# Optimization experiments

Measured on AMD Instinct MI355X. Metric: run time of the kernel, lower is better.

## Reference

```python
import jax, jax.numpy as jnp
import numpy as np

N_NODES = 50000
N_EDGES = 640000
IN_DIM = 128
HID = 128
G_OUT = 128
AX_IN = 64
AX_OUT = 64
OUT_CH = 8
N_GRAPHS = 512


def gcn_conv(x, W, b, src, dst, norm, n_nodes):
    # PyG GCNConv: out = scatter_add(norm * (x W)[src] -> dst) + b
    h = x @ W  # [N, F_out]
    msg = h[src] * norm[:, None]  # [E', F_out]
    return jax.ops.segment_sum(msg, dst, num_segments=n_nodes) + b


def setup_inputs() -> dict:
    key = jax.random.key(0)
    ks = jax.random.split(key, 16)
    inp = {}
    inp["x"] = jax.random.normal(ks[0], (N_NODES, IN_DIM), dtype=jnp.float32)
    inp["edge_index"] = jax.random.randint(ks[1], (2, N_EDGES), 0, N_NODES, dtype=jnp.int64)
    inp["batch"] = jnp.sort(jax.random.randint(ks[2], (N_NODES,), 0, N_GRAPHS, dtype=jnp.int64))
    inp["ax_data"] = jax.random.normal(ks[3], (N_GRAPHS, AX_IN), dtype=jnp.float32)
    def lin(k, fi, fo):
        s = 1.0 / np.sqrt(fi)
        k1, k2 = jax.random.split(k)
        return (jax.random.uniform(k1, (fi, fo), jnp.float32, -s, s),
                jax.random.uniform(k2, (fo,), jnp.float32, -s, s))
    inp["W1"], inp["b1"] = lin(ks[4], IN_DIM, HID)
    inp["W2"], inp["b2"] = lin(ks[5], HID, HID)
    inp["lin1_W"], inp["lin1_b"] = lin(ks[6], HID, G_OUT)
    inp["ax_W"], inp["ax_b"] = lin(ks[7], AX_IN, AX_OUT)
    inp["lin2_W"], inp["lin2_b"] = lin(ks[8], G_OUT + AX_OUT, OUT_CH)
    return inp


def reference(x, edge_index, batch, ax_data, W1, b1, W2, b2, lin1_W, lin1_b, ax_W, ax_b, lin2_W, lin2_b):
    n_nodes = x.shape[0]
    n_graphs = ax_data.shape[0]
    # add self-loops (PyG GCNConv default add_self_loops=True)
    loop = jnp.arange(n_nodes, dtype=edge_index.dtype)
    src = jnp.concatenate([edge_index[0], loop])
    dst = jnp.concatenate([edge_index[1], loop])
    # symmetric normalization D^-1/2 (A+I) D^-1/2
    deg = jax.ops.segment_sum(jnp.ones_like(dst, dtype=x.dtype), dst, num_segments=n_nodes)
    dinv = jax.lax.rsqrt(jnp.maximum(deg, 1.0))  # deg >= 1 with self-loops
    norm = dinv[src] * dinv[dst]  # [E+N]

    h = jax.nn.relu(gcn_conv(x, W1, b1, src, dst, norm, n_nodes))
    h = jax.nn.relu(gcn_conv(h, W2, b2, src, dst, norm, n_nodes))

    # global_mean_pool over batch ids
    sums = jax.ops.segment_sum(h, batch, num_segments=n_graphs)
    cnts = jax.ops.segment_sum(jnp.ones((n_nodes,), h.dtype), batch, num_segments=n_graphs)
    pooled = sums / jnp.maximum(cnts, 1.0)[:, None]  # [G, HID]

    g = pooled @ lin1_W + lin1_b            # [G, G_OUT]
    a = ax_data @ ax_W + ax_b               # [G, AX_OUT]
    z = jnp.concatenate([g, a], axis=1)     # [G, G_OUT+AX_OUT]
    return z @ lin2_W + lin2_b              # [G, OUT_CH]
```

## Files before the change

kernel.cpp:

```cpp
#include <hip/hip_runtime.h>


#define ELLCAP 62
#define BCAP 2048

typedef __attribute__((ext_vector_type(8))) short bf16x8;
typedef __attribute__((ext_vector_type(4))) float f32x4;
typedef __attribute__((ext_vector_type(2))) float f32x2;

static __device__ __forceinline__ unsigned short f2bf(float f) {
  unsigned u = __float_as_uint(f);
  return (unsigned short)((u + 0x7fffu + ((u >> 16) & 1u)) >> 16);
}
static __device__ __forceinline__ unsigned pack2(float a, float b) {
  return (unsigned)f2bf(a) | ((unsigned)f2bf(b) << 16);
}
static __device__ __forceinline__ unsigned char f2fp8(float v) {
  return (unsigned char)(__builtin_amdgcn_cvt_pk_fp8_f32(v, 0.f, 0, false) & 0xff);
}
static __device__ __forceinline__ unsigned enc2(float a, float b) {
  return __builtin_amdgcn_cvt_pk_fp8_f32(a, b, 0, false) & 0xffffu;
}
static __device__ __forceinline__ void add16(float* a, uint4 h) {
  f32x2 t;
  t = __builtin_amdgcn_cvt_pk_f32_fp8(h.x, false); a[0] += t[0]; a[1] += t[1];
  t = __builtin_amdgcn_cvt_pk_f32_fp8(h.x, true);  a[2] += t[0]; a[3] += t[1];
  t = __builtin_amdgcn_cvt_pk_f32_fp8(h.y, false); a[4] += t[0]; a[5] += t[1];
  t = __builtin_amdgcn_cvt_pk_f32_fp8(h.y, true);  a[6] += t[0]; a[7] += t[1];
  t = __builtin_amdgcn_cvt_pk_f32_fp8(h.z, false); a[8] += t[0]; a[9] += t[1];
  t = __builtin_amdgcn_cvt_pk_f32_fp8(h.z, true);  a[10] += t[0]; a[11] += t[1];
  t = __builtin_amdgcn_cvt_pk_f32_fp8(h.w, false); a[12] += t[0]; a[13] += t[1];
  t = __builtin_amdgcn_cvt_pk_f32_fp8(h.w, true);  a[14] += t[0]; a[15] += t[1];
}
static __device__ __forceinline__ uint4 scale16(uint4 h, float d) {
  f32x2 t; float v[16];
  t = __builtin_amdgcn_cvt_pk_f32_fp8(h.x, false); v[0] = d * t[0]; v[1] = d * t[1];
  t = __builtin_amdgcn_cvt_pk_f32_fp8(h.x, true);  v[2] = d * t[0]; v[3] = d * t[1];
  t = __builtin_amdgcn_cvt_pk_f32_fp8(h.y, false); v[4] = d * t[0]; v[5] = d * t[1];
  t = __builtin_amdgcn_cvt_pk_f32_fp8(h.y, true);  v[6] = d * t[0]; v[7] = d * t[1];
  t = __builtin_amdgcn_cvt_pk_f32_fp8(h.z, false); v[8] = d * t[0]; v[9] = d * t[1];
  t = __builtin_amdgcn_cvt_pk_f32_fp8(h.z, true);  v[10] = d * t[0]; v[11] = d * t[1];
  t = __builtin_amdgcn_cvt_pk_f32_fp8(h.w, false); v[12] = d * t[0]; v[13] = d * t[1];
  t = __builtin_amdgcn_cvt_pk_f32_fp8(h.w, true);  v[14] = d * t[0]; v[15] = d * t[1];
  uint4 r;
  r.x = enc2(v[0], v[1]) | (enc2(v[2], v[3]) << 16);
  r.y = enc2(v[4], v[5]) | (enc2(v[6], v[7]) << 16);
  r.z = enc2(v[8], v[9]) | (enc2(v[10], v[11]) << 16);
  r.w = enc2(v[12], v[13]) | (enc2(v[14], v[15]) << 16);
  return r;
}

__global__ void k_wprep(const float* __restrict__ W1, const float* __restrict__ W2,
                        unsigned short* __restrict__ wt1, unsigned short* __restrict__ wt2,
                        unsigned* __restrict__ gcnt, int nb) {
  int b = blockIdx.x, t = threadIdx.x;
  if (b < 128) {
    int idx = b * 256 + t;
    int w = idx >> 14, r = (idx >> 7) & 127, kk = idx & 127;
    if (w == 0) wt1[r * 128 + kk] = f2bf(W1[kk * 128 + r]);
    else        wt2[r * 128 + kk] = f2bf(W2[kk * 128 + r]);
  } else {
    int i = (b - 128) * 256 + t;
    if (i < nb) gcnt[i * 32] = 0;
  }
}

__global__ __launch_bounds__(256, 4) void k_mega1(
    const float* __restrict__ X, const uint4* __restrict__ WT4,
    unsigned char* __restrict__ H8,
    const int* __restrict__ srcv, const int* __restrict__ dstv,
    unsigned* __restrict__ gcnt, unsigned* __restrict__ packed,
    int E, int M, int NG) {
  __shared__ __align__(16) unsigned short sW[64 * 136];
  __shared__ __align__(16) unsigned short sX[64 * 136];
  __shared__ unsigned sbin[392];
  __shared__ unsigned sbase[392];
  int b = blockIdx.x, t = threadIdx.x;
  if (b < NG) {
    int m0 = b * 64;
    const float4* X4 = (const float4*)X;
#pragma unroll
    for (int r = 0; r < 8; r++) {
      int idx = t + r * 256;
      int rr = idx >> 5, c4 = idx & 31;
      int m = m0 + rr;
      float4 v = make_float4(0.f, 0.f, 0.f, 0.f);
      if (m < M) v = X4[(size_t)m * 32 + c4];
      unsigned short* pp = sX + rr * 136 + c4 * 4;
      *(ushort2*)(pp) = make_ushort2(f2bf(v.x), f2bf(v.y));
      *(ushort2*)(pp + 2) = make_ushort2(f2bf(v.z), f2bf(v.w));
    }
    int lane = t & 63, wv = t >> 6;
    int ln15 = lane & 15, q = lane >> 4;
    int r0 = m0 + wv * 16 + q * 4;
    bf16x8 afrag[4];
#pragma unroll
    for (int half = 0; half < 2; half++) {
      if (half) __syncthreads();
#pragma unroll
      for (int r = 0; r < 4; r++) {
        int idx = t + r * 256;
        int nn = idx >> 4, c8 = idx & 15;
        *(uint4*)(sW + nn * 136 + c8 * 8) = WT4[(half * 64 + nn) * 16 + c8];
      }
      __syncthreads();
      if (half == 0) {
#pragma unroll
        for (int c = 0; c < 4; c++)
          afrag[c] = *(const bf16x8*)(sX + (wv * 16 + ln15) * 136 + c * 32 + q * 8);
      }
#pragma unroll
      for (int jj = 0; jj < 4; jj++) {
        int j = half * 4 + jj;
        f32x4 acc = {0.f, 0.f, 0.f, 0.f};
#pragma unroll
        for (int c = 0; c < 4; c++) {
          bf16x8 bfrag = *(const bf16x8*)(sW + (jj * 16 + ln15) * 136 + c * 32 + q * 8);
          acc = __builtin_amdgcn_mfma_f32_16x16x32_bf16(afrag[c], bfrag, acc, 0, 0, 0);
        }
        int col = j * 16 + ln15;
#pragma unroll
        for (int rr = 0; rr < 4; rr++) {
          int m = r0 + rr;
          if (m < M) H8[(size_t)m * 128 + col] = f2fp8(acc[rr]);
        }
      }
    }
  } else {
    int NB = (M + 127) >> 7;
    int e0 = (b - NG) * BCAP;
    int myS[8], myD[8];
#pragma unroll
    for (int j = 0; j < 8; j++) {
      int e = e0 + t + j * 256;
      if (e < E) { myS[j] = srcv[e]; myD[j] = dstv[e]; } else myD[j] = -1;
    }
    for (int i = t; i < NB; i += 256) sbin[i] = 0;
    __syncthreads();
#pragma unroll
    for (int j = 0; j < 8; j++)
      if (myD[j] >= 0) atomicAdd(&sbin[myD[j] >> 7], 1u);
    __syncthreads();
    for (int i = t; i < NB; i += 256) {
      unsigned c = sbin[i];
      sbase[i] = c ? atomicAdd(&gcnt[i * 32], c) : 0u;
    }
    __syncthreads();
    for (int i = t; i < NB; i += 256) sbin[i] = 0;
    __syncthreads();
#pragma unroll
    for (int j = 0; j < 8; j++)
      if (myD[j] >= 0) {
        int bkt = myD[j] >> 7;
        unsigned r = atomicAdd(&sbin[bkt], 1u);
        unsigned pos = sbase[bkt] + r;
        if (pos < BCAP)
          packed[(size_t)bkt * BCAP + pos] =
              (unsigned)myS[j] | ((unsigned)(myD[j] & 127) << 16);
      }
  }
}

__global__ __launch_bounds__(256) void k_ellbuild(const unsigned* __restrict__ packed,
                                                  const unsigned* __restrict__ gcnt,
                                                  unsigned char* __restrict__ ellb,
                                                  uint4* __restrict__ H8,
                                                  float* __restrict__ dinv,
                                                  int n) {
  __shared__ unsigned short ent[128][ELLCAP];
  __shared__ int ctr[128];
  __shared__ int scnt;
  int b = blockIdx.x, t = threadIdx.x;
  if (t < 128) ctr[t] = 0;
  if (t == 0) scnt = (int)gcnt[b * 32];
  __syncthreads();
  int cnt = scnt; if (cnt > BCAP) cnt = BCAP;
  const unsigned* pk = packed + (size_t)b * BCAP;
  for (int idx = t; idx < cnt; idx += 256) {
    unsigned v = pk[idx];
    int dloc = (int)(v >> 16);
    int slot = atomicAdd(&ctr[dloc], 1);
    if (slot < ELLCAP) ent[dloc][slot] = (unsigned short)(v & 0xffffu);
  }
  __syncthreads();
  int base = b * 128;
#pragma unroll
  for (int p = 0; p < 16; p++) {
    int idx = t + p * 256;
    int i = idx >> 5, u = idx & 31;
    int node = base + i;
    if (node < n) {
      unsigned val;
      if (u == 0) val = (unsigned)ctr[i];
      else {
        int e0 = 2 * u - 2;
        val = (unsigned)ent[i][e0] | ((unsigned)ent[i][e0 + 1] << 16);
      }
      ((unsigned*)ellb)[(size_t)node * 32 + u] = val;
    }
  }
#pragma unroll
  for (int p = 0; p < 4; p++) {
    int idx = t + p * 256;
    int i2 = idx >> 3, kk = idx & 7;
    int node = base + i2;
    if (node < n) {
      float di = rsqrtf((float)(ctr[i2] + 1));
      uint4 h = H8[(size_t)node * 8 + kk];
      H8[(size_t)node * 8 + kk] = scale16(h, di);
      if (kk == 0) dinv[node] = di;
    }
  }
}

#define EXTR(S, wa, wb, wc, wd, J)                                     \
  {                                                                    \
    S[0] = (int)((wa) & 0xffffu); S[1] = (int)((wa) >> 16);            \
    S[2] = (int)((wb) & 0xffffu); S[3] = (int)((wb) >> 16);            \
    S[4] = (int)((wc) & 0xffffu); S[5] = (int)((wc) >> 16);            \
    S[6] = (int)((wd) & 0xffffu); S[7] = (int)((wd) >> 16);            \
    _Pragma("unroll")                                                  \
    for (int u_ = 1; u_ < 8; u_++)                                     \
      if ((J) + u_ >= deg) S[u_] = S[0];                               \
  }
#define GATHER(H, S)                                                   \
  _Pragma("unroll")                                                    \
  for (int u_ = 0; u_ < 8; u_++) H[u_] = Hs[(size_t)S[u_] * 8 + k];
#define CONSUME(H, J)                                                  \
  _Pragma("unroll")                                                    \
  for (int u_ = 0; u_ < 8; u_++)                                       \
    if ((J) + u_ < deg) add16(acc, H[u_]);

__global__ __launch_bounds__(256) void k_agg(const uint4* __restrict__ Hs,
                                             const unsigned char* __restrict__ ellb,
                                             const float* __restrict__ dinv,
                                             const float* __restrict__ bias,
                                             uint4* __restrict__ Ho, int n) {
  int t = threadIdx.x;
  int oct = t >> 3, k = t & 7;
  int i = blockIdx.x * 32 + oct;
  bool valid = i < n;
  int ic = valid ? i : 0;
  const uint4* rp = (const uint4*)(ellb + (size_t)ic * 128);
  uint4 q0 = rp[0], q1 = rp[1], q2 = rp[2], q3 = rp[3];
  uint4 hs = Hs[(size_t)ic * 8 + k];
  float di = dinv[ic];
  int raw = (int)q0.x;
  int deg = raw < ELLCAP ? raw : ELLCAP;
  float acc[16];
#pragma unroll
  for (int r = 0; r < 16; r++) acc[r] = 0.f;
  int sA[8], sB[8], sC[8];
  uint4 hA[8], hB[8], hC[8];
  if (deg > 0)  { EXTR(sA, q0.y, q0.z, q0.w, q1.x, 0);  GATHER(hA, sA); }
  if (deg > 8)  { EXTR(sB, q1.y, q1.z, q1.w, q2.x, 8);  GATHER(hB, sB); }
  if (deg > 16) { EXTR(sC, q2.y, q2.z, q2.w, q3.x, 16); GATHER(hC, sC); }
  uint4 q4 = make_uint4(0u, 0u, 0u, 0u), q5 = q4, q6 = q4, q7 = q4;
  if (deg > 24) { q4 = rp[4]; q5 = rp[5]; q6 = rp[6]; q7 = rp[7]; }
  add16(acc, hs);
  if (deg > 0)  CONSUME(hA, 0);
  if (deg > 24) { EXTR(sA, q3.y, q3.z, q3.w, q4.x, 24); GATHER(hA, sA); }
  if (deg > 8)  CONSUME(hB, 8);
  if (deg > 32) { EXTR(sB, q4.y, q4.z, q4.w, q5.x, 32); GATHER(hB, sB); }
  if (deg > 16) CONSUME(hC, 16);
  if (deg > 40) { EXTR(sC, q5.y, q5.z, q5.w, q6.x, 40); GATHER(hC, sC); }
  if (deg > 24) CONSUME(hA, 24);
  if (deg > 48) { EXTR(sA, q6.y, q6.z, q6.w, q7.x, 48); GATHER(hA, sA); }
  if (deg > 32) CONSUME(hB, 32);
  if (deg > 56) { EXTR(sB, q7.y, q7.z, q7.w, q7.w, 56); GATHER(hB, sB); }
  if (deg > 40) CONSUME(hC, 40);
  if (deg > 48) CONSUME(hA, 48);
  if (deg > 56) CONSUME(hB, 56);
  if (valid) {
    const float4* B4 = (const float4*)bias;
    float o[16];
#pragma unroll
    for (int m4 = 0; m4 < 4; m4++) {
      float4 bb = B4[k * 4 + m4];
      o[m4 * 4 + 0] = fmaxf(bb.x + di * acc[m4 * 4 + 0], 0.f);
      o[m4 * 4 + 1] = fmaxf(bb.y + di * acc[m4 * 4 + 1], 0.f);
      o[m4 * 4 + 2] = fmaxf(bb.z + di * acc[m4 * 4 + 2], 0.f);
      o[m4 * 4 + 3] = fmaxf(bb.w + di * acc[m4 * 4 + 3], 0.f);
    }
    uint4 r0, r1;
    r0.x = pack2(o[0], o[1]);   r0.y = pack2(o[2], o[3]);
    r0.z = pack2(o[4], o[5]);   r0.w = pack2(o[6], o[7]);
    r1.x = pack2(o[8], o[9]);   r1.y = pack2(o[10], o[11]);
    r1.z = pack2(o[12], o[13]); r1.w = pack2(o[14], o[15]);
    Ho[(size_t)i * 16 + 2 * k] = r0;
    Ho[(size_t)i * 16 + 2 * k + 1] = r1;
  }
}

__global__ __launch_bounds__(256, 2) void k_gemm2(const unsigned short* __restrict__ Xb,
                                                  const uint4* __restrict__ WT4,
                                                  const float* __restrict__ dinv,
                                                  unsigned char* __restrict__ H8, int M) {
  __shared__ __align__(16) unsigned short sW[128 * 136];
  __shared__ __align__(16) unsigned short sX[64 * 136];
  int tid = threadIdx.x;
  int m0 = blockIdx.x * 64;
#pragma unroll
  for (int r = 0; r < 8; r++) {
    int idx = tid + r * 256;
    int nn = idx >> 4, c8 = idx & 15;
    *(uint4*)(sW + nn * 136 + c8 * 8) = WT4[idx];
  }
  const uint4* X4 = (const uint4*)Xb;
#pragma unroll
  for (int r = 0; r < 4; r++) {
    int idx = tid + r * 256;
    int rr = idx >> 4, c8 = idx & 15;
    int m = m0 + rr;
    uint4 v = make_uint4(0u, 0u, 0u, 0u);
    if (m < M) v = X4[(size_t)m * 16 + c8];
    *(uint4*)(sX + rr * 136 + c8 * 8) = v;
  }
  __syncthreads();
  int lane = tid & 63, wv = tid >> 6;
  int ln15 = lane & 15, q = lane >> 4;
  bf16x8 afrag[4];
#pragma unroll
  for (int c = 0; c < 4; c++)
    afrag[c] = *(const bf16x8*)(sX + (wv * 16 + ln15) * 136 + c * 32 + q * 8);
  int r0 = m0 + wv * 16 + q * 4;
  float dv[4];
#pragma unroll
  for (int rr = 0; rr < 4; rr++) dv[rr] = (r0 + rr < M) ? dinv[r0 + rr] : 0.f;
#pragma unroll
  for (int j = 0; j < 8; j++) {
    f32x4 acc = {0.f, 0.f, 0.f, 0.f};
#pragma unroll
    for (int c = 0; c < 4; c++) {
      bf16x8 bfrag = *(const bf16x8*)(sW + (j * 16 + ln15) * 136 + c * 32 + q * 8);
      acc = __builtin_amdgcn_mfma_f32_16x16x32_bf16(afrag[c], bfrag, acc, 0, 0, 0);
    }
    int col = j * 16 + ln15;
#pragma unroll
    for (int rr = 0; rr < 4; rr++) {
      int m = r0 + rr;
      if (m < M) H8[(size_t)m * 128 + col] = f2fp8(dv[rr] * acc[rr]);
    }
  }
}

__global__ void k_poolhead(const unsigned short* __restrict__ Hb,
                           const int* __restrict__ bat, const float* __restrict__ axd,
                           const float* __restrict__ l1W, const float* __restrict__ l1b,
                           const float* __restrict__ axW, const float* __restrict__ axb,
                           const float* __restrict__ l2W, const float* __restrict__ l2b,
                           float* __restrict__ out, int n) {
  int g = blockIdx.x, t = threadIdx.x;
  __shared__ int sb[2];
  __shared__ float p[128];
  __shared__ float a[64];
  __shared__ float z[192];
  if (t < 2) {
    int target = g + t;
    int lo = 0, hi = n;
    while (lo < hi) {
      int mid = (lo + hi) >> 1;
      if (bat[mid] < target) lo = mid + 1; else hi = mid;
    }
    sb[t] = lo;
  }
  __syncthreads();
  int s = sb[0], e = sb[1];
  int c = e - s; if (c < 1) c = 1;
  float inv = 1.f / (float)c;
  if (t < 128) {
    float s0 = 0.f, s1 = 0.f, s2 = 0.f, s3 = 0.f;
    float s4 = 0.f, s5 = 0.f, s6 = 0.f, s7 = 0.f;
    int r = s;
    for (; r + 8 <= e; r += 8) {
      s0 += __uint_as_float(((unsigned)Hb[(size_t)(r + 0) * 128 + t]) << 16);
      s1 += __uint_as_float(((unsigned)Hb[(size_t)(r + 1) * 128 + t]) << 16);
      s2 += __uint_as_float(((unsigned)Hb[(size_t)(r + 2) * 128 + t]) << 16);
      s3 += __uint_as_float(((unsigned)Hb[(size_t)(r + 3) * 128 + t]) << 16);
      s4 += __uint_as_float(((unsigned)Hb[(size_t)(r + 4) * 128 + t]) << 16);
      s5 += __uint_as_float(((unsigned)Hb[(size_t)(r + 5) * 128 + t]) << 16);
      s6 += __uint_as_float(((unsigned)Hb[(size_t)(r + 6) * 128 + t]) << 16);
      s7 += __uint_as_float(((unsigned)Hb[(size_t)(r + 7) * 128 + t]) << 16);
    }
    for (; r < e; r++)
      s0 += __uint_as_float(((unsigned)Hb[(size_t)r * 128 + t]) << 16);
    p[t] = (((s0 + s1) + (s2 + s3)) + ((s4 + s5) + (s6 + s7))) * inv;
  } else {
    a[t - 128] = axd[g * 64 + (t - 128)];
  }
  __syncthreads();
  if (t < 128) {
    float a0 = 0.f, a1 = 0.f, a2 = 0.f, a3 = 0.f;
#pragma unroll 8
    for (int kk = 0; kk < 128; kk += 4) {
      a0 += p[kk + 0] * l1W[(kk + 0) * 128 + t];
      a1 += p[kk + 1] * l1W[(kk + 1) * 128 + t];
      a2 += p[kk + 2] * l1W[(kk + 2) * 128 + t];
      a3 += p[kk + 3] * l1W[(kk + 3) * 128 + t];
    }
    z[t] = l1b[t] + (a0 + a1) + (a2 + a3);
  } else {
    int j = t - 128;
    float a0 = 0.f, a1 = 0.f, a2 = 0.f, a3 = 0.f;
#pragma unroll 8
    for (int kk = 0; kk < 64; kk += 4) {
      a0 += a[kk + 0] * axW[(kk + 0) * 64 + j];
      a1 += a[kk + 1] * axW[(kk + 1) * 64 + j];
      a2 += a[kk + 2] * axW[(kk + 2) * 64 + j];
      a3 += a[kk + 3] * axW[(kk + 3) * 64 + j];
    }
    z[128 + j] = axb[j] + (a0 + a1) + (a2 + a3);
  }
  __syncthreads();
  if (t < 8) {
    float a0 = 0.f, a1 = 0.f, a2 = 0.f, a3 = 0.f;
#pragma unroll 8
    for (int kk = 0; kk < 192; kk += 4) {
      a0 += z[kk + 0] * l2W[(kk + 0) * 8 + t];
      a1 += z[kk + 1] * l2W[(kk + 1) * 8 + t];
      a2 += z[kk + 2] * l2W[(kk + 2) * 8 + t];
      a3 += z[kk + 3] * l2W[(kk + 3) * 8 + t];
    }
    out[g * 8 + t] = l2b[t] + (a0 + a1) + (a2 + a3);
  }
}

extern "C" void kernel_launch(void* const* d_in, const int* in_sizes, int n_in,
                              void* d_out, int out_size, void* d_ws, size_t ws_size,
                              hipStream_t stream) {
  const float* x   = (const float*)d_in[0];
  const int*   ei  = (const int*)d_in[1];
  const int*   bat = (const int*)d_in[2];
  const float* axd = (const float*)d_in[3];
  const float* W1  = (const float*)d_in[4];
  const float* b1  = (const float*)d_in[5];
  const float* W2  = (const float*)d_in[6];
  const float* b2  = (const float*)d_in[7];
  const float* l1W = (const float*)d_in[8];
  const float* l1b = (const float*)d_in[9];
  const float* axW = (const float*)d_in[10];
  const float* axb = (const float*)d_in[11];
  const float* l2W = (const float*)d_in[12];
  const float* l2b = (const float*)d_in[13];
  float* out = (float*)d_out;

  int n = in_sizes[0] / 128;
  int E = in_sizes[1] / 2;
  int G = in_sizes[3] / 64;
  (void)G;
  int NB = (n + 127) / 128;

  unsigned char* w = (unsigned char*)d_ws;
  unsigned char*  h8    = w;                     w += (size_t)n * 128;
  unsigned short* habuf = (unsigned short*)w;    w += (size_t)n * 128 * 2;
  unsigned short* wt1   = (unsigned short*)w;    w += 16384 * 2;
  unsigned short* wt2   = (unsigned short*)w;    w += 16384 * 2;
  unsigned char*  ellb  = w;                     w += (size_t)n * 128;
  float*    dinv   = (float*)w;                  w += (size_t)n * 4;
  unsigned* gcnt   = (unsigned*)w;               w += (size_t)NB * 128;
  unsigned* packed = (unsigned*)w;               w += (size_t)NB * BCAP * 4;

  const int* srcv = ei;
  const int* dstv = ei + E;
  int NG = (n + 63) / 64;
  int NPB = (E + BCAP - 1) / BCAP;
  int GZ = (NB + 255) / 256;

  k_wprep<<<128 + GZ, 256, 0, stream>>>(W1, W2, wt1, wt2, gcnt, NB);
  k_mega1<<<NG + NPB, 256, 0, stream>>>(x, (const uint4*)wt1, h8, srcv, dstv,
                                        gcnt, packed, E, n, NG);
  k_ellbuild<<<NB, 256, 0, stream>>>(packed, gcnt, ellb, (uint4*)h8, dinv, n);
  k_agg<<<(n + 31) / 32, 256, 0, stream>>>((const uint4*)h8, ellb, dinv, b1,
                                           (uint4*)habuf, n);
  k_gemm2<<<NG, 256, 0, stream>>>(habuf, (const uint4*)wt2, dinv, h8, n);
  k_agg<<<(n + 31) / 32, 256, 0, stream>>>((const uint4*)h8, ellb, dinv, b2,
                                           (uint4*)habuf, n);
  k_poolhead<<<512, 192, 0, stream>>>(habuf, bat, axd, l1W, l1b, axW, axb,
                                      l2W, l2b, out, n);
}
```

Measured before the change: 186.3 us.

## Shrink k_agg gather pipeline to two buffers, raise occupancy, nontemporal stores

Reworks the ELL aggregation kernel to keep only two in-flight gather buffers instead of three and to handle high-degree rows with a runtime loop that reads index words directly, instead of fully unrolled code with extra prefetched index vectors. Launch bounds now request 4 blocks per SM so the lower register footprint can buy occupancy. Output stores become nontemporal. The trade is less memory-level parallelism per thread, and a serialized load-then-consume loop for high-degree nodes, in exchange for more resident waves.

```diff
diff --git a/kernel.cpp b/kernel.cpp
--- a/kernel.cpp
+++ b/kernel.cpp
@@ -7,6 +7,7 @@
 typedef __attribute__((ext_vector_type(8))) short bf16x8;
 typedef __attribute__((ext_vector_type(4))) float f32x4;
 typedef __attribute__((ext_vector_type(2))) float f32x2;
+typedef __attribute__((ext_vector_type(4))) unsigned int u32x4;
 
 static __device__ __forceinline__ unsigned short f2bf(float f) {
   unsigned u = __float_as_uint(f);
@@ -213,29 +214,31 @@
   }
 }
 
-#define EXTR(S, wa, wb, wc, wd, J)                                     \
-  {                                                                    \
-    S[0] = (int)((wa) & 0xffffu); S[1] = (int)((wa) >> 16);            \
-    S[2] = (int)((wb) & 0xffffu); S[3] = (int)((wb) >> 16);            \
-    S[4] = (int)((wc) & 0xffffu); S[5] = (int)((wc) >> 16);            \
-    S[6] = (int)((wd) & 0xffffu); S[7] = (int)((wd) >> 16);            \
-    _Pragma("unroll")                                                  \
-    for (int u_ = 1; u_ < 8; u_++)                                     \
-      if ((J) + u_ >= deg) S[u_] = S[0];                               \
-  }
-#define GATHER(H, S)                                                   \
-  _Pragma("unroll")                                                    \
-  for (int u_ = 0; u_ < 8; u_++) H[u_] = Hs[(size_t)S[u_] * 8 + k];
-#define CONSUME(H, J)                                                  \
-  _Pragma("unroll")                                                    \
-  for (int u_ = 0; u_ < 8; u_++)                                       \
+#define GLOAD(H, wa, wb, wc, wd, J)                                          \
+  {                                                                          \
+    int i0_ = (int)((wa) & 0xffffu), i1_ = (int)((wa) >> 16);                \
+    int i2_ = (int)((wb) & 0xffffu), i3_ = (int)((wb) >> 16);                \
+    int i4_ = (int)((wc) & 0xffffu), i5_ = (int)((wc) >> 16);                \
+    int i6_ = (int)((wd) & 0xffffu), i7_ = (int)((wd) >> 16);                \
+    if ((J) + 0 >= deg) i0_ = s0;  if ((J) + 1 >= deg) i1_ = s0;             \
+    if ((J) + 2 >= deg) i2_ = s0;  if ((J) + 3 >= deg) i3_ = s0;             \
+    if ((J) + 4 >= deg) i4_ = s0;  if ((J) + 5 >= deg) i5_ = s0;             \
+    if ((J) + 6 >= deg) i6_ = s0;  if ((J) + 7 >= deg) i7_ = s0;             \
+    H[0] = Hs[(size_t)i0_ * 8 + k]; H[1] = Hs[(size_t)i1_ * 8 + k];          \
+    H[2] = Hs[(size_t)i2_ * 8 + k]; H[3] = Hs[(size_t)i3_ * 8 + k];          \
+    H[4] = Hs[(size_t)i4_ * 8 + k]; H[5] = Hs[(size_t)i5_ * 8 + k];          \
+    H[6] = Hs[(size_t)i6_ * 8 + k]; H[7] = Hs[(size_t)i7_ * 8 + k];          \
+  }
+#define CONSUME(H, J)                                                        \
+  _Pragma("unroll")                                                          \
+  for (int u_ = 0; u_ < 8; u_++)                                             \
     if ((J) + u_ < deg) add16(acc, H[u_]);
 
-__global__ __launch_bounds__(256) void k_agg(const uint4* __restrict__ Hs,
-                                             const unsigned char* __restrict__ ellb,
-                                             const float* __restrict__ dinv,
-                                             const float* __restrict__ bias,
-                                             uint4* __restrict__ Ho, int n) {
+__global__ __launch_bounds__(256, 4) void k_agg(const uint4* __restrict__ Hs,
+                                                const unsigned char* __restrict__ ellb,
+                                                const float* __restrict__ dinv,
+                                                const float* __restrict__ bias,
+                                                uint4* __restrict__ Ho, int n) {
   int t = threadIdx.x;
   int oct = t >> 3, k = t & 7;
   int i = blockIdx.x * 32 + oct;
@@ -247,30 +250,33 @@
   float di = dinv[ic];
   int raw = (int)q0.x;
   int deg = raw < ELLCAP ? raw : ELLCAP;
+  int s0 = (int)(q0.y & 0xffffu);
   float acc[16];
 #pragma unroll
   for (int r = 0; r < 16; r++) acc[r] = 0.f;
-  int sA[8], sB[8], sC[8];
-  uint4 hA[8], hB[8], hC[8];
-  if (deg > 0)  { EXTR(sA, q0.y, q0.z, q0.w, q1.x, 0);  GATHER(hA, sA); }
-  if (deg > 8)  { EXTR(sB, q1.y, q1.z, q1.w, q2.x, 8);  GATHER(hB, sB); }
-  if (deg > 16) { EXTR(sC, q2.y, q2.z, q2.w, q3.x, 16); GATHER(hC, sC); }
-  uint4 q4 = make_uint4(0u, 0u, 0u, 0u), q5 = q4, q6 = q4, q7 = q4;
-  if (deg > 24) { q4 = rp[4]; q5 = rp[5]; q6 = rp[6]; q7 = rp[7]; }
+  uint4 hA[8], hB[8];
+  if (deg > 0)  GLOAD(hA, q0.y, q0.z, q0.w, q1.x, 0);
+  if (deg > 8)  GLOAD(hB, q1.y, q1.z, q1.w, q2.x, 8);
   add16(acc, hs);
   if (deg > 0)  CONSUME(hA, 0);
-  if (deg > 24) { EXTR(sA, q3.y, q3.z, q3.w, q4.x, 24); GATHER(hA, sA); }
+  if (deg > 16) GLOAD(hA, q2.y, q2.z, q2.w, q3.x, 16);
   if (deg > 8)  CONSUME(hB, 8);
-  if (deg > 32) { EXTR(sB, q4.y, q4.z, q4.w, q5.x, 32); GATHER(hB, sB); }
-  if (deg > 16) CONSUME(hC, 16);
-  if (deg > 40) { EXTR(sC, q5.y, q5.z, q5.w, q6.x, 40); GATHER(hC, sC); }
-  if (deg > 24) CONSUME(hA, 24);
-  if (deg > 48) { EXTR(sA, q6.y, q6.z, q6.w, q7.x, 48); GATHER(hA, sA); }
-  if (deg > 32) CONSUME(hB, 32);
-  if (deg > 56) { EXTR(sB, q7.y, q7.z, q7.w, q7.w, 56); GATHER(hB, sB); }
-  if (deg > 40) CONSUME(hC, 40);
-  if (deg > 48) CONSUME(hA, 48);
-  if (deg > 56) CONSUME(hB, 56);
+  if (deg > 24) {
+    const unsigned* wp = (const unsigned*)(ellb + (size_t)ic * 128 + 4);
+    {
+      unsigned wa = wp[12], wb = wp[13], wc = wp[14], wd = wp[15];
+      GLOAD(hB, wa, wb, wc, wd, 24);
+    }
+    if (deg > 16) CONSUME(hA, 16);
+    CONSUME(hB, 24);
+    for (int j = 32; j < deg; j += 8) {
+      unsigned wa = wp[j / 2], wb = wp[j / 2 + 1], wc = wp[j / 2 + 2], wd = wp[j / 2 + 3];
+      GLOAD(hA, wa, wb, wc, wd, j);
+      CONSUME(hA, j);
+    }
+  } else {
+    if (deg > 16) CONSUME(hA, 16);
+  }
   if (valid) {
     const float4* B4 = (const float4*)bias;
     float o[16];
@@ -282,13 +288,13 @@
       o[m4 * 4 + 2] = fmaxf(bb.z + di * acc[m4 * 4 + 2], 0.f);
       o[m4 * 4 + 3] = fmaxf(bb.w + di * acc[m4 * 4 + 3], 0.f);
     }
-    uint4 r0, r1;
-    r0.x = pack2(o[0], o[1]);   r0.y = pack2(o[2], o[3]);
-    r0.z = pack2(o[4], o[5]);   r0.w = pack2(o[6], o[7]);
-    r1.x = pack2(o[8], o[9]);   r1.y = pack2(o[10], o[11]);
-    r1.z = pack2(o[12], o[13]); r1.w = pack2(o[14], o[15]);
-    Ho[(size_t)i * 16 + 2 * k] = r0;
-    Ho[(size_t)i * 16 + 2 * k + 1] = r1;
+    u32x4 r0, r1;
+    r0[0] = pack2(o[0], o[1]);   r0[1] = pack2(o[2], o[3]);
+    r0[2] = pack2(o[4], o[5]);   r0[3] = pack2(o[6], o[7]);
+    r1[0] = pack2(o[8], o[9]);   r1[1] = pack2(o[10], o[11]);
+    r1[2] = pack2(o[12], o[13]); r1[3] = pack2(o[14], o[15]);
+    __builtin_nontemporal_store(r0, (u32x4*)&Ho[(size_t)i * 16 + 2 * k]);
+    __builtin_nontemporal_store(r1, (u32x4*)&Ho[(size_t)i * 16 + 2 * k + 1]);
   }
 }
 
```

Result: slower. 193.0 us (+3.6%).
